# Optimization experiments

Measured on AMD Instinct MI355X. Metric: run time of the kernel, lower is better.

## Reference

```python
import jax, jax.numpy as jnp
import numpy as np

METRIC = [1.0, 1.0, 1.0, 0.0]  # Cl(3,0,1) projective geometric algebra
N_BLADES = 1 << len(METRIC)    # 16
BATCH = 2097152


def _build_cayley(metric):
    """Cayley structure-constant tensor C[i,j,k]: (a b)_k = sum_ij a_i b_j C[i,j,k].
    Blades indexed by bitmask over generators; e_A e_B = sign * e_{A xor B}."""
    d = len(metric)
    n = 1 << d
    cay = np.zeros((n, n, n), dtype=np.float32)
    for A in range(n):
        for B in range(n):
            # canonical reordering sign (count transpositions)
            sa, s = A >> 1, 0
            while sa:
                s += bin(sa & B).count("1")
                sa >>= 1
            sign = -1.0 if (s & 1) else 1.0
            # contract common generators through the metric
            for i in range(d):
                if A & B & (1 << i):
                    sign *= metric[i]
            if sign != 0.0:
                cay[A, B, A ^ B] = sign
    return cay


def setup_inputs() -> dict:
    key = jax.random.key(0)
    k1, k2 = jax.random.split(key)
    a = jax.random.normal(k1, (BATCH, N_BLADES), dtype=jnp.float32)
    b = jax.random.normal(k2, (BATCH, N_BLADES), dtype=jnp.float32)
    cayley = jnp.asarray(_build_cayley(METRIC))  # [16,16,16], sparse structure constants
    return {"a": a, "b": b, "cayley": cayley}


def reference(a, b, cayley):
    # Geometric product: (a b)_k = sum_{i,j} a_i b_j C[i,j,k]
    a = a.astype(jnp.float32)
    b = b.astype(jnp.float32)
    return jnp.einsum("...i,ijk,...j->...k", a, cayley, b)
```

## Files before the change

kernel.cpp:

```cpp
#include <hip/hip_runtime.h>


__host__ __device__ constexpr float cayley_sign(int A, int B) {
    int s = 0;
    for (int sa = A >> 1; sa; sa >>= 1) s += __builtin_popcount(sa & B);
    float sign = (s & 1) ? -1.0f : 1.0f;
    if (A & B & 8) sign = 0.0f;
    return sign;
}

__device__ __forceinline__ int swz(int f) {
    return (f & ~3) | ((f ^ (f >> 3)) & 3);
}

__global__ void __launch_bounds__(256)
gp_cl301_kernel(const float4* __restrict__ a4,
                const float4* __restrict__ b4,
                float4* __restrict__ o4) {
    __shared__ float4 lds_a[1024];
    __shared__ float4 lds_b[1024];

    const int i = threadIdx.x;
    const long tile_f4 = (long)blockIdx.x * 1024;

    float4 ra[4], rb[4];
    #pragma unroll
    for (int q = 0; q < 4; ++q) {
        ra[q] = a4[tile_f4 + q * 256 + i];
        rb[q] = b4[tile_f4 + q * 256 + i];
    }
    #pragma unroll
    for (int q = 0; q < 4; ++q) {
        const int s = swz(q * 256 + i);
        lds_a[s] = ra[q];
        lds_b[s] = rb[q];
    }
    __syncthreads();

    float A[16], B[16];
    #pragma unroll
    for (int c = 0; c < 4; ++c) {
        const int s = i * 4 + (c ^ ((i >> 1) & 3));
        const float4 va = lds_a[s];
        const float4 vb = lds_b[s];
        A[c*4+0] = va.x; A[c*4+1] = va.y; A[c*4+2] = va.z; A[c*4+3] = va.w;
        B[c*4+0] = vb.x; B[c*4+1] = vb.y; B[c*4+2] = vb.z; B[c*4+3] = vb.w;
    }

    float O[16] = {0,0,0,0, 0,0,0,0, 0,0,0,0, 0,0,0,0};
    #pragma unroll
    for (int ii = 0; ii < 16; ++ii) {
        #pragma unroll
        for (int jj = 0; jj < 16; ++jj) {
            const float s = cayley_sign(ii, jj);
            if (s != 0.0f) {
                O[ii ^ jj] += s * A[ii] * B[jj];
            }
        }
    }

    #pragma unroll
    for (int c = 0; c < 4; ++c) {
        const int s = i * 4 + (c ^ ((i >> 1) & 3));
        lds_a[s] = make_float4(O[c*4+0], O[c*4+1], O[c*4+2], O[c*4+3]);
    }
    __syncthreads();

    #pragma unroll
    for (int q = 0; q < 4; ++q) {
        const int f = q * 256 + i;
        o4[tile_f4 + f] = lds_a[swz(f)];
    }
}

extern "C" void kernel_launch(void* const* d_in, const int* in_sizes, int n_in,
                              void* d_out, int out_size, void* d_ws, size_t ws_size,
                              hipStream_t stream) {
    const float4* a4 = (const float4*)d_in[0];
    const float4* b4 = (const float4*)d_in[1];
    float4* o4 = (float4*)d_out;

    const int n = in_sizes[0] / 16;
    const int tiles = n / 256;

    gp_cl301_kernel<<<tiles, 256, 0, stream>>>(a4, b4, o4);
}
```

Baseline: 75.90 us.

## Use per-wave persistent tiles with direct global-to-LDS loads and nontemporal stores

Restructures the kernel so each wave owns a private 64-row LDS slice and loops persistently over tiles on a fixed 2048-block grid. Inputs are loaded with global_load_lds (swizzled source addresses) instead of going through registers, and outputs use nontemporal stores. Block-wide __syncthreads are gone because each wave only touches its own slice. The aim is less register staging, no block barriers and less cache pollution. The cost is that loads and compute inside a wave are serialized by vmcnt(0) waits, with no double buffering.

```diff
diff --git a/kernel.cpp b/kernel.cpp
--- a/kernel.cpp
+++ b/kernel.cpp
@@ -9,67 +9,82 @@
     return sign;
 }
 
-__device__ __forceinline__ int swz(int f) {
-    return (f & ~3) | ((f ^ (f >> 3)) & 3);
+__device__ __forceinline__ int swz(int p) {
+    return (p & ~3) | ((p ^ (p >> 3)) & 3);
 }
+
+typedef float vfloat4 __attribute__((ext_vector_type(4)));
 
 __global__ void __launch_bounds__(256)
 gp_cl301_kernel(const float4* __restrict__ a4,
                 const float4* __restrict__ b4,
-                float4* __restrict__ o4) {
-    __shared__ float4 lds_a[1024];
-    __shared__ float4 lds_b[1024];
+                float4* __restrict__ o4,
+                int ntiles) {
+    __shared__ float4 lds[4][2][256];
 
-    const int i = threadIdx.x;
-    const long tile_f4 = (long)blockIdx.x * 1024;
+    const int l = threadIdx.x & 63;
+    const int w = threadIdx.x >> 6;
+    float4* sl_a = &lds[w][0][0];
+    float4* sl_b = &lds[w][1][0];
 
-    float4 ra[4], rb[4];
-    #pragma unroll
-    for (int q = 0; q < 4; ++q) {
-        ra[q] = a4[tile_f4 + q * 256 + i];
-        rb[q] = b4[tile_f4 + q * 256 + i];
-    }
-    #pragma unroll
-    for (int q = 0; q < 4; ++q) {
-        const int s = swz(q * 256 + i);
-        lds_a[s] = ra[q];
-        lds_b[s] = rb[q];
-    }
-    __syncthreads();
+    const int wave_id = blockIdx.x * 4 + w;
+    const int nwaves  = gridDim.x * 4;
 
-    float A[16], B[16];
-    #pragma unroll
-    for (int c = 0; c < 4; ++c) {
-        const int s = i * 4 + (c ^ ((i >> 1) & 3));
-        const float4 va = lds_a[s];
-        const float4 vb = lds_b[s];
-        A[c*4+0] = va.x; A[c*4+1] = va.y; A[c*4+2] = va.z; A[c*4+3] = va.w;
-        B[c*4+0] = vb.x; B[c*4+1] = vb.y; B[c*4+2] = vb.z; B[c*4+3] = vb.w;
-    }
+    for (int t = wave_id; t < ntiles; t += nwaves) {
+        const long base = (long)t * 256;
 
-    float O[16] = {0,0,0,0, 0,0,0,0, 0,0,0,0, 0,0,0,0};
-    #pragma unroll
-    for (int ii = 0; ii < 16; ++ii) {
+        asm volatile("s_waitcnt lgkmcnt(0)" ::: "memory");
+
         #pragma unroll
-        for (int jj = 0; jj < 16; ++jj) {
-            const float s = cayley_sign(ii, jj);
-            if (s != 0.0f) {
-                O[ii ^ jj] += s * A[ii] * B[jj];
+        for (int q = 0; q < 4; ++q) {
+            const int ps = swz(q * 64 + l);
+            __builtin_amdgcn_global_load_lds(
+                (const __attribute__((address_space(1))) void*)(a4 + base + ps),
+                (__attribute__((address_space(3))) void*)(sl_a + q * 64),
+                16, 0, 0);
+            __builtin_amdgcn_global_load_lds(
+                (const __attribute__((address_space(1))) void*)(b4 + base + ps),
+                (__attribute__((address_space(3))) void*)(sl_b + q * 64),
+                16, 0, 0);
+        }
+        asm volatile("s_waitcnt vmcnt(0)" ::: "memory");
+        __builtin_amdgcn_sched_barrier(0);
+
+        float A[16], B[16];
+        #pragma unroll
+        for (int c = 0; c < 4; ++c) {
+            const int s = l * 4 + (c ^ ((l >> 1) & 3));
+            const float4 va = sl_a[s];
+            const float4 vb = sl_b[s];
+            A[c*4+0] = va.x; A[c*4+1] = va.y; A[c*4+2] = va.z; A[c*4+3] = va.w;
+            B[c*4+0] = vb.x; B[c*4+1] = vb.y; B[c*4+2] = vb.z; B[c*4+3] = vb.w;
+        }
+
+        float O[16] = {0,0,0,0, 0,0,0,0, 0,0,0,0, 0,0,0,0};
+        #pragma unroll
+        for (int ii = 0; ii < 16; ++ii) {
+            #pragma unroll
+            for (int jj = 0; jj < 16; ++jj) {
+                const float s = cayley_sign(ii, jj);
+                if (s != 0.0f) {
+                    O[ii ^ jj] += s * A[ii] * B[jj];
+                }
             }
         }
-    }
 
-    #pragma unroll
-    for (int c = 0; c < 4; ++c) {
-        const int s = i * 4 + (c ^ ((i >> 1) & 3));
-        lds_a[s] = make_float4(O[c*4+0], O[c*4+1], O[c*4+2], O[c*4+3]);
-    }
-    __syncthreads();
+        #pragma unroll
+        for (int c = 0; c < 4; ++c) {
+            const int s = l * 4 + (c ^ ((l >> 1) & 3));
+            sl_a[s] = make_float4(O[c*4+0], O[c*4+1], O[c*4+2], O[c*4+3]);
+        }
 
-    #pragma unroll
-    for (int q = 0; q < 4; ++q) {
-        const int f = q * 256 + i;
-        o4[tile_f4 + f] = lds_a[swz(f)];
+        #pragma unroll
+        for (int q = 0; q < 4; ++q) {
+            const int p = q * 64 + l;
+            float4 v = sl_a[swz(p)];
+            __builtin_nontemporal_store(*(const vfloat4*)&v,
+                                        (vfloat4*)(o4 + base + p));
+        }
     }
 }
 
@@ -80,8 +95,9 @@
     const float4* b4 = (const float4*)d_in[1];
     float4* o4 = (float4*)d_out;
 
-    const int n = in_sizes[0] / 16;
-    const int tiles = n / 256;
+    const int n      = in_sizes[0] / 16;
+    const int ntiles = n / 64;
 
-    gp_cl301_kernel<<<tiles, 256, 0, stream>>>(a4, b4, o4);
+    const int grid = 2048;
+    gp_cl301_kernel<<<grid, 256, 0, stream>>>(a4, b4, o4, ntiles);
 }
```

After: 62.47 us, median of 2. 17.7% less time.
